# Kernel tuning notes

Measured on AMD Instinct MI355X. Metric: run time of the kernel, lower is better.

Reference implementation:

```python
import jax, jax.numpy as jnp
import numpy as np

STATE_DIM = 2
HIDDEN = 1024
N_SKILLS = 5
N_ACTIONS = 4
BATCH = 65536


def setup_inputs() -> dict:
    key = jax.random.key(0)
    ks = jax.random.split(key, 8)
    def lin_init(k, fan_in, shape):
        bound = 1.0 / np.sqrt(fan_in)
        return jax.random.uniform(k, shape, jnp.float32, -bound, bound)
    return {
        "s": jax.random.normal(ks[0], (BATCH, STATE_DIM), jnp.float32),
        "skill_idx": jax.random.randint(ks[1], (BATCH,), 0, N_SKILLS, jnp.int32),
        "W1": lin_init(ks[2], STATE_DIM, (STATE_DIM, HIDDEN)),
        "b1": lin_init(ks[3], STATE_DIM, (HIDDEN,)),
        "W2": lin_init(ks[4], HIDDEN, (HIDDEN, HIDDEN)),
        "b2": lin_init(ks[5], HIDDEN, (HIDDEN,)),
        "W_heads": lin_init(ks[6], HIDDEN, (N_SKILLS, HIDDEN, N_ACTIONS)),
        "b_heads": lin_init(ks[7], HIDDEN, (N_SKILLS, N_ACTIONS)),
    }


def reference(s, skill_idx, W1, b1, W2, b2, W_heads, b_heads):
    # shared feature MLP: Linear -> ReLU -> Linear -> ReLU
    h = jax.nn.relu(s @ W1 + b1)            # [B, H]
    feat = jax.nn.relu(h @ W2 + b2)         # [B, H]
    # per-sample skill head: gather weights then one batched contraction
    Wg = W_heads[skill_idx]                 # [B, H, A]
    bg = b_heads[skill_idx]                 # [B, A]
    return jnp.einsum('bh,bha->ba', feat, Wg) + bg  # [B, A]
```

## Files before the change

### kernel.cpp

```cpp
#include <hip/hip_runtime.h>

typedef __bf16 bf16x8 __attribute__((ext_vector_type(8)));
typedef __bf16 bf16x4 __attribute__((ext_vector_type(4)));
typedef float  floatx4 __attribute__((ext_vector_type(4)));

#define GLOBAL_AS __attribute__((address_space(1)))
#define LOCAL_AS  __attribute__((address_space(3)))

static constexpr int HID = 1024;
static constexpr int MT  = 128;
static constexpr int BK  = 64;
static constexpr int KIT = HID / BK;

__device__ __forceinline__ void h8(bf16x8& d, float s0, float s1,
                                   const float4& w0a, const float4& w0b,
                                   const float4& w1a, const float4& w1b,
                                   const float4& ba,  const float4& bb) {
    d[0] = (__bf16)fmaxf(fmaf(s1, w1a.x, fmaf(s0, w0a.x, ba.x)), 0.f);
    d[1] = (__bf16)fmaxf(fmaf(s1, w1a.y, fmaf(s0, w0a.y, ba.y)), 0.f);
    d[2] = (__bf16)fmaxf(fmaf(s1, w1a.z, fmaf(s0, w0a.z, ba.z)), 0.f);
    d[3] = (__bf16)fmaxf(fmaf(s1, w1a.w, fmaf(s0, w0a.w, ba.w)), 0.f);
    d[4] = (__bf16)fmaxf(fmaf(s1, w1b.x, fmaf(s0, w0b.x, bb.x)), 0.f);
    d[5] = (__bf16)fmaxf(fmaf(s1, w1b.y, fmaf(s0, w0b.y, bb.y)), 0.f);
    d[6] = (__bf16)fmaxf(fmaf(s1, w1b.z, fmaf(s0, w0b.z, bb.z)), 0.f);
    d[7] = (__bf16)fmaxf(fmaf(s1, w1b.w, fmaf(s0, w0b.w, bb.w)), 0.f);
}

__global__ __launch_bounds__(256)
void prep_all(const float* __restrict__ S,  const float* __restrict__ W1,
              const float* __restrict__ B1, const float* __restrict__ W2,
              const float* __restrict__ WH,
              __bf16* __restrict__ H, __bf16* __restrict__ W2T,
              __bf16* __restrict__ WHT, float* __restrict__ OUT,
              int row0, int nh, int nz) {
    if (blockIdx.x < (unsigned)nh) {
        const int wid  = blockIdx.x * 4 + (threadIdx.x >> 6);
        const int lane = threadIdx.x & 63;
        const int rb   = wid * 8;
        const int c0   = lane * 8;
        const float4 w0a0 = *(const float4*)(W1 + c0);
        const float4 w0b0 = *(const float4*)(W1 + c0 + 4);
        const float4 w1a0 = *(const float4*)(W1 + HID + c0);
        const float4 w1b0 = *(const float4*)(W1 + HID + c0 + 4);
        const float4 ba0  = *(const float4*)(B1 + c0);
        const float4 bb0  = *(const float4*)(B1 + c0 + 4);
        const float4 w0a1 = *(const float4*)(W1 + 512 + c0);
        const float4 w0b1 = *(const float4*)(W1 + 512 + c0 + 4);
        const float4 w1a1 = *(const float4*)(W1 + HID + 512 + c0);
        const float4 w1b1 = *(const float4*)(W1 + HID + 512 + c0 + 4);
        const float4 ba1  = *(const float4*)(B1 + 512 + c0);
        const float4 bb1  = *(const float4*)(B1 + 512 + c0 + 4);
        float2 sv[8];
#pragma unroll
        for (int r = 0; r < 8; ++r)
            sv[r] = *(const float2*)(S + (size_t)(row0 + rb + r) * 2);
#pragma unroll
        for (int r = 0; r < 8; ++r) {
            const int rl = rb + r;
            const int xo = ((((c0 >> 3) & 7) ^ (rl & 7)) << 3);
            bf16x8 hv0, hv1;
            h8(hv0, sv[r].x, sv[r].y, w0a0, w0b0, w1a0, w1b0, ba0, bb0);
            h8(hv1, sv[r].x, sv[r].y, w0a1, w0b1, w1a1, w1b1, ba1, bb1);
            *(bf16x8*)(H + (size_t)rl * HID + ((c0 & ~63) | xo))       = hv0;
            *(bf16x8*)(H + (size_t)rl * HID + ((c0 & ~63) | xo) + 512) = hv1;
        }
        return;
    }
    int b = blockIdx.x - nh;
    if (b < nz) {
        ((float4*)OUT)[(size_t)row0 + (size_t)b * 256 + threadIdx.x]
            = make_float4(0.f, 0.f, 0.f, 0.f);
        return;
    }
    b -= nz;
    if (b < 256) {
        __shared__ __bf16 tile[64][65];
        const int bx = b & 15;
        const int by = b >> 4;
        const int a  = threadIdx.x & 63;
        const int bb = threadIdx.x >> 6;
#pragma unroll
        for (int r = 0; r < 16; ++r) {
            const int k = r * 4 + bb;
            tile[a][k] = (__bf16)W2[(size_t)(by * 64 + k) * HID + bx * 64 + a];
        }
        __syncthreads();
#pragma unroll
        for (int r = 0; r < 16; ++r) {
            const int n = r * 4 + bb;
            const int g = a >> 3, j = a & 7;
            const int ksw = ((g ^ (n & 7)) << 3) | j;
            W2T[(size_t)(bx * 64 + n) * HID + by * 64 + ksw] = tile[n][a];
        }
    } else {
        const int r = b - 256;
        const int s = r >> 2, a = r & 3;
        for (int k = threadIdx.x; k < HID; k += 256) {
            const float v = (r < 20) ? WH[((size_t)s * HID + k) * 4 + a] : 0.f;
            const int c = k >> 7, o = (k >> 3) & 15, j = k & 7;
            const int sw = (o & 8) | ((o & 7) ^ (r & 7));
            WHT[(size_t)r * HID + c * 128 + sw * 8 + j] = (__bf16)v;
        }
    }
}

__global__ __launch_bounds__(256, 4)
void policy_main(const __bf16* __restrict__ H, const int* __restrict__ SK,
                 const __bf16* __restrict__ W2T, const float* __restrict__ B2,
                 const __bf16* __restrict__ WHT, const float* __restrict__ BH,
                 float* __restrict__ OUT, int row0, int mg_bits) {
    __shared__ __align__(16) char smem[40960];
    __bf16* hA    = (__bf16*)smem;
    __bf16* Bt    = (__bf16*)(smem + 16384);
    __bf16* featL = (__bf16*)smem;
    __bf16* WHTL  = (__bf16*)(smem + 32768);

    const int tid  = threadIdx.x;
    const int lane = tid & 63;
    const int wv   = tid >> 6;
    const int wm   = wv & 1;
    const int wn   = wv >> 1;
    const int l15  = lane & 15;
    const int quad = lane >> 4;
    const int n8   = blockIdx.x >> mg_bits;
    const int i0l  = (blockIdx.x & ((1 << mg_bits) - 1)) * MT;

    floatx4 acc[4][4] = {};
    floatx4 hacc[2][2] = {};

#pragma unroll
    for (int c = 0; c < 2; ++c) {
        const int rb = c * 16 + wv * 4;
        const __bf16* gp = WHT + (size_t)(rb + (lane >> 4)) * HID
                         + n8 * 128 + (lane & 15) * 8;
        __builtin_amdgcn_global_load_lds((GLOBAL_AS void*)gp,
                                         (LOCAL_AS void*)(WHTL + rb * 128), 16, 0, 0);
    }

#pragma unroll 1
    for (int kt = 0; kt < KIT; ++kt) {
        __syncthreads();
#pragma unroll
        for (int c = 0; c < 4; ++c) {
            const int rb = c * 32 + wv * 8;
            const __bf16* gp = H + (size_t)(i0l + rb + (lane >> 3)) * HID
                             + kt * BK + (lane & 7) * 8;
            __builtin_amdgcn_global_load_lds((GLOBAL_AS void*)gp,
                                             (LOCAL_AS void*)(hA + rb * 64), 16, 0, 0);
        }
#pragma unroll
        for (int c = 0; c < 4; ++c) {
            const int rb = c * 32 + wv * 8;
            const __bf16* gp = W2T + (size_t)(n8 * 128 + rb + (lane >> 3)) * HID
                             + kt * BK + (lane & 7) * 8;
            __builtin_amdgcn_global_load_lds((GLOBAL_AS void*)gp,
                                             (LOCAL_AS void*)(Bt + rb * 64), 16, 0, 0);
        }
        __syncthreads();
#pragma unroll
        for (int ks = 0; ks < 2; ++ks) {
            bf16x8 wf[4], hf[4];
#pragma unroll
            for (int f = 0; f < 4; ++f) {
                const int row = wn * 64 + f * 16 + l15;
                wf[f] = *(const bf16x8*)(Bt + row * 64 + (((ks * 4 + quad) ^ (row & 7)) * 8));
            }
#pragma unroll
            for (int f = 0; f < 4; ++f) {
                const int smp = wm * 64 + f * 16 + l15;
                hf[f] = *(const bf16x8*)(hA + smp * 64 + (((ks * 4 + quad) ^ (smp & 7)) * 8));
            }
#pragma unroll
            for (int fn = 0; fn < 4; ++fn)
#pragma unroll
                for (int fm = 0; fm < 4; ++fm)
                    acc[fn][fm] = __builtin_amdgcn_mfma_f32_16x16x32_bf16(
                        wf[fn], hf[fm], acc[fn][fm], 0, 0, 0);
        }
    }

    __syncthreads();
#pragma unroll
    for (int fn = 0; fn < 4; ++fn) {
        const int fcb = wn * 64 + fn * 16 + quad * 4;
        const float4 b2v = *(const float4*)(B2 + n8 * 128 + fcb);
#pragma unroll
        for (int fm = 0; fm < 4; ++fm) {
            const int smp = wm * 64 + fm * 16 + l15;
            const floatx4 v = acc[fn][fm];
            bf16x4 p;
            p[0] = (__bf16)fmaxf(v[0] + b2v.x, 0.f);
            p[1] = (__bf16)fmaxf(v[1] + b2v.y, 0.f);
            p[2] = (__bf16)fmaxf(v[2] + b2v.z, 0.f);
            p[3] = (__bf16)fmaxf(v[3] + b2v.w, 0.f);
            *(bf16x4*)(featL + smp * 128 + (((fcb >> 3) ^ (smp & 15)) << 3) + (fcb & 7)) = p;
        }
    }
    __syncthreads();

#pragma unroll
    for (int f2 = 0; f2 < 2; ++f2) {
#pragma unroll
        for (int ks2 = 0; ks2 < 4; ++ks2) {
            const int row = wv * 32 + f2 * 16 + l15;
            const bf16x8 fa = *(const bf16x8*)(featL + row * 128
                                 + (((ks2 * 4 + quad) ^ (row & 15)) << 3));
#pragma unroll
            for (int t2 = 0; t2 < 2; ++t2) {
                const int r = t2 * 16 + l15;
                const int o = ks2 * 4 + quad;
                const int sw = (o & 8) | ((o & 7) ^ (r & 7));
                const bf16x8 wb = *(const bf16x8*)(WHTL + r * 128 + sw * 8);
                hacc[f2][t2] = __builtin_amdgcn_mfma_f32_16x16x32_bf16(
                    fa, wb, hacc[f2][t2], 0, 0, 0);
            }
        }
    }

#pragma unroll
    for (int f2 = 0; f2 < 2; ++f2)
#pragma unroll
        for (int j = 0; j < 4; ++j) {
            const int smp = wv * 32 + f2 * 16 + quad * 4 + j;
            const int sk  = SK[(size_t)row0 + i0l + smp];
#pragma unroll
            for (int t2 = 0; t2 < 2; ++t2) {
                const int hc = t2 * 16 + l15;
                const int d  = hc - sk * 4;
                if (d >= 0 && d < 4) {
                    float v = hacc[f2][t2][j];
                    if (n8 == 0) v += BH[hc];
                    atomicAdd(&OUT[(size_t)(row0 + i0l + smp) * 4 + d], v);
                }
            }
        }
}

extern "C" void kernel_launch(void* const* d_in, const int* in_sizes, int n_in,
                              void* d_out, int out_size, void* d_ws, size_t ws_size,
                              hipStream_t stream) {
    const float* S  = (const float*)d_in[0];
    const int*   SK = (const int*)d_in[1];
    const float* W1 = (const float*)d_in[2];
    const float* B1 = (const float*)d_in[3];
    const float* W2 = (const float*)d_in[4];
    const float* B2 = (const float*)d_in[5];
    const float* WH = (const float*)d_in[6];
    const float* BH = (const float*)d_in[7];

    char* ws = (char*)d_ws;
    __bf16* W2T = (__bf16*)ws;
    __bf16* WHT = (__bf16*)(ws + 2 * 1024 * 1024);
    __bf16* H   = (__bf16*)(ws + 2 * 1024 * 1024 + 65536);

    const size_t fixed = 2 * 1024 * 1024 + 65536;
    const size_t avail = ws_size > fixed ? ws_size - fixed : 0;
    int nc = 1;
    while (nc < 64 && (size_t)(65536 / nc) * HID * sizeof(__bf16) > avail) nc <<= 1;
    const int Mc = 65536 / nc;
    int mg_bits = 0;
    while ((1 << mg_bits) < Mc / MT) ++mg_bits;

    for (int c = 0; c < nc; ++c) {
        const int nh = Mc / 32;
        const int nz = Mc / 256;
        const int extra = (c == 0) ? 288 : 0;
        hipLaunchKernelGGL(prep_all, dim3(nh + nz + extra), dim3(256), 0, stream,
                           S, W1, B1, W2, WH, H, W2T, WHT, (float*)d_out,
                           c * Mc, nh, nz);
        hipLaunchKernelGGL(policy_main, dim3((Mc / MT) * 8), dim3(256), 0, stream,
                           H, SK, W2T, B2, WHT, BH, (float*)d_out, c * Mc, mg_bits);
    }
}
```

Before: 249.9 us.

## Fuse first layer into GEMM main loop, dropping materialized H buffer

The first Linear+ReLU is no longer computed by a prep pass that writes a bf16 H matrix (65536x1024) to workspace. The main GEMM kernel now computes each 64-column K-slice of H on the fly from S, W1 and B1 and writes it into LDS. The chunking logic is gone and the kernel always handles the full batch. This removes a 128 MB write and the matching reads, but each of the 8 N-blocks per row tile recomputes H, adding ALU work and global W1/B1 loads inside the K loop.

```diff
diff --git a/kernel.cpp b/kernel.cpp
--- a/kernel.cpp
+++ b/kernel.cpp
@@ -27,52 +27,16 @@
 }
 
 __global__ __launch_bounds__(256)
-void prep_all(const float* __restrict__ S,  const float* __restrict__ W1,
-              const float* __restrict__ B1, const float* __restrict__ W2,
-              const float* __restrict__ WH,
-              __bf16* __restrict__ H, __bf16* __restrict__ W2T,
-              __bf16* __restrict__ WHT, float* __restrict__ OUT,
-              int row0, int nh, int nz) {
-    if (blockIdx.x < (unsigned)nh) {
-        const int wid  = blockIdx.x * 4 + (threadIdx.x >> 6);
-        const int lane = threadIdx.x & 63;
-        const int rb   = wid * 8;
-        const int c0   = lane * 8;
-        const float4 w0a0 = *(const float4*)(W1 + c0);
-        const float4 w0b0 = *(const float4*)(W1 + c0 + 4);
-        const float4 w1a0 = *(const float4*)(W1 + HID + c0);
-        const float4 w1b0 = *(const float4*)(W1 + HID + c0 + 4);
-        const float4 ba0  = *(const float4*)(B1 + c0);
-        const float4 bb0  = *(const float4*)(B1 + c0 + 4);
-        const float4 w0a1 = *(const float4*)(W1 + 512 + c0);
-        const float4 w0b1 = *(const float4*)(W1 + 512 + c0 + 4);
-        const float4 w1a1 = *(const float4*)(W1 + HID + 512 + c0);
-        const float4 w1b1 = *(const float4*)(W1 + HID + 512 + c0 + 4);
-        const float4 ba1  = *(const float4*)(B1 + 512 + c0);
-        const float4 bb1  = *(const float4*)(B1 + 512 + c0 + 4);
-        float2 sv[8];
-#pragma unroll
-        for (int r = 0; r < 8; ++r)
-            sv[r] = *(const float2*)(S + (size_t)(row0 + rb + r) * 2);
-#pragma unroll
-        for (int r = 0; r < 8; ++r) {
-            const int rl = rb + r;
-            const int xo = ((((c0 >> 3) & 7) ^ (rl & 7)) << 3);
-            bf16x8 hv0, hv1;
-            h8(hv0, sv[r].x, sv[r].y, w0a0, w0b0, w1a0, w1b0, ba0, bb0);
-            h8(hv1, sv[r].x, sv[r].y, w0a1, w0b1, w1a1, w1b1, ba1, bb1);
-            *(bf16x8*)(H + (size_t)rl * HID + ((c0 & ~63) | xo))       = hv0;
-            *(bf16x8*)(H + (size_t)rl * HID + ((c0 & ~63) | xo) + 512) = hv1;
-        }
-        return;
-    }
-    int b = blockIdx.x - nh;
-    if (b < nz) {
-        ((float4*)OUT)[(size_t)row0 + (size_t)b * 256 + threadIdx.x]
+void prep_all(const float* __restrict__ W2, const float* __restrict__ WH,
+              __bf16* __restrict__ W2T, __bf16* __restrict__ WHT,
+              float* __restrict__ OUT) {
+    int b = blockIdx.x;
+    if (b < 256) {
+        ((float4*)OUT)[(size_t)b * 256 + threadIdx.x]
             = make_float4(0.f, 0.f, 0.f, 0.f);
         return;
     }
-    b -= nz;
+    b -= 256;
     if (b < 256) {
         __shared__ __bf16 tile[64][65];
         const int bx = b & 15;
@@ -105,10 +69,11 @@
 }
 
 __global__ __launch_bounds__(256, 4)
-void policy_main(const __bf16* __restrict__ H, const int* __restrict__ SK,
+void policy_main(const float* __restrict__ S,  const int* __restrict__ SK,
+                 const float* __restrict__ W1, const float* __restrict__ B1,
                  const __bf16* __restrict__ W2T, const float* __restrict__ B2,
                  const __bf16* __restrict__ WHT, const float* __restrict__ BH,
-                 float* __restrict__ OUT, int row0, int mg_bits) {
+                 float* __restrict__ OUT) {
     __shared__ __align__(16) char smem[40960];
     __bf16* hA    = (__bf16*)smem;
     __bf16* Bt    = (__bf16*)(smem + 16384);
@@ -122,8 +87,11 @@
     const int wn   = wv >> 1;
     const int l15  = lane & 15;
     const int quad = lane >> 4;
-    const int n8   = blockIdx.x >> mg_bits;
-    const int i0l  = (blockIdx.x & ((1 << mg_bits) - 1)) * MT;
+    const int n8   = blockIdx.x >> 9;
+    const int i0l  = (blockIdx.x & 511) * MT;
+
+    const int a8  = lane & 7;
+    const int oct = lane >> 3;
 
     floatx4 acc[4][4] = {};
     floatx4 hacc[2][2] = {};
@@ -137,17 +105,14 @@
                                          (LOCAL_AS void*)(WHTL + rb * 128), 16, 0, 0);
     }
 
+    float2 sv[4];
+#pragma unroll
+    for (int k = 0; k < 4; ++k)
+        sv[k] = *(const float2*)(S + (size_t)(i0l + wv * 32 + a8 + 8 * k) * 2);
+
 #pragma unroll 1
     for (int kt = 0; kt < KIT; ++kt) {
         __syncthreads();
-#pragma unroll
-        for (int c = 0; c < 4; ++c) {
-            const int rb = c * 32 + wv * 8;
-            const __bf16* gp = H + (size_t)(i0l + rb + (lane >> 3)) * HID
-                             + kt * BK + (lane & 7) * 8;
-            __builtin_amdgcn_global_load_lds((GLOBAL_AS void*)gp,
-                                             (LOCAL_AS void*)(hA + rb * 64), 16, 0, 0);
-        }
 #pragma unroll
         for (int c = 0; c < 4; ++c) {
             const int rb = c * 32 + wv * 8;
@@ -155,6 +120,21 @@
                              + kt * BK + (lane & 7) * 8;
             __builtin_amdgcn_global_load_lds((GLOBAL_AS void*)gp,
                                              (LOCAL_AS void*)(Bt + rb * 64), 16, 0, 0);
+        }
+        {
+            const float4 w0a = *(const float4*)(W1 + kt * BK + oct * 8);
+            const float4 w0b = *(const float4*)(W1 + kt * BK + oct * 8 + 4);
+            const float4 w1a = *(const float4*)(W1 + HID + kt * BK + oct * 8);
+            const float4 w1b = *(const float4*)(W1 + HID + kt * BK + oct * 8 + 4);
+            const float4 ba  = *(const float4*)(B1 + kt * BK + oct * 8);
+            const float4 bb  = *(const float4*)(B1 + kt * BK + oct * 8 + 4);
+#pragma unroll
+            for (int k = 0; k < 4; ++k) {
+                const int smp = wv * 32 + a8 + 8 * k;
+                bf16x8 hv;
+                h8(hv, sv[k].x, sv[k].y, w0a, w0b, w1a, w1b, ba, bb);
+                *(bf16x8*)(hA + smp * 64 + ((oct ^ a8) << 3)) = hv;
+            }
         }
         __syncthreads();
 #pragma unroll
@@ -222,7 +202,7 @@
 #pragma unroll
         for (int j = 0; j < 4; ++j) {
             const int smp = wv * 32 + f2 * 16 + quad * 4 + j;
-            const int sk  = SK[(size_t)row0 + i0l + smp];
+            const int sk  = SK[(size_t)i0l + smp];
 #pragma unroll
             for (int t2 = 0; t2 < 2; ++t2) {
                 const int hc = t2 * 16 + l15;
@@ -230,7 +210,7 @@
                 if (d >= 0 && d < 4) {
                     float v = hacc[f2][t2][j];
                     if (n8 == 0) v += BH[hc];
-                    atomicAdd(&OUT[(size_t)(row0 + i0l + smp) * 4 + d], v);
+                    atomicAdd(&OUT[(size_t)(i0l + smp) * 4 + d], v);
                 }
             }
         }
@@ -251,24 +231,9 @@
     char* ws = (char*)d_ws;
     __bf16* W2T = (__bf16*)ws;
     __bf16* WHT = (__bf16*)(ws + 2 * 1024 * 1024);
-    __bf16* H   = (__bf16*)(ws + 2 * 1024 * 1024 + 65536);
-
-    const size_t fixed = 2 * 1024 * 1024 + 65536;
-    const size_t avail = ws_size > fixed ? ws_size - fixed : 0;
-    int nc = 1;
-    while (nc < 64 && (size_t)(65536 / nc) * HID * sizeof(__bf16) > avail) nc <<= 1;
-    const int Mc = 65536 / nc;
-    int mg_bits = 0;
-    while ((1 << mg_bits) < Mc / MT) ++mg_bits;
-
-    for (int c = 0; c < nc; ++c) {
-        const int nh = Mc / 32;
-        const int nz = Mc / 256;
-        const int extra = (c == 0) ? 288 : 0;
-        hipLaunchKernelGGL(prep_all, dim3(nh + nz + extra), dim3(256), 0, stream,
-                           S, W1, B1, W2, WH, H, W2T, WHT, (float*)d_out,
-                           c * Mc, nh, nz);
-        hipLaunchKernelGGL(policy_main, dim3((Mc / MT) * 8), dim3(256), 0, stream,
-                           H, SK, W2T, B2, WHT, BH, (float*)d_out, c * Mc, mg_bits);
-    }
-}
+
+    hipLaunchKernelGGL(prep_all, dim3(256 + 256 + 32), dim3(256), 0, stream,
+                       W2, WH, W2T, WHT, (float*)d_out);
+    hipLaunchKernelGGL(policy_main, dim3((65536 / MT) * 8), dim3(256), 0, stream,
+                       S, SK, W1, B1, W2T, B2, WHT, BH, (float*)d_out);
+}
```

After: 229.8 us. 8.0% less time.
